# Kernel tuning notes

Hardware: AMD Instinct MI355X
Metric: run time of the kernel (lower is better)

The kernel has to match this reference:

```python
import jax, jax.numpy as jnp
import numpy as np

D_MODEL = 768
NHEAD = 12
DK = D_MODEL // NHEAD
MAX_DIST = 1000.0
FF = 3072
POS_HIDDEN = 32  # hidden width of the relative-position bias MLP
EPS = 1e-5
B, L = 2, 1024


def setup_inputs() -> dict:
    key = jax.random.key(0)
    ks = jax.random.split(key, 24)

    def lin(k, i, o):  # torch-Linear-like init, stored as (in, out)
        return jax.random.uniform(k, (i, o), jnp.float32, -1.0, 1.0) / np.sqrt(i)

    return {
        "src": jax.random.normal(ks[0], (B, L, D_MODEL), jnp.float32),
        "src_x": jax.random.uniform(ks[1], (B, L), jnp.float32) * 1000.0,
        "src_y": jax.random.uniform(ks[2], (B, L), jnp.float32) * 1000.0,
        # attention projections (q,k,v,out)
        "Wq": lin(ks[3], D_MODEL, D_MODEL), "bq": jnp.zeros((D_MODEL,), jnp.float32),
        "Wk": lin(ks[4], D_MODEL, D_MODEL), "bk": jnp.zeros((D_MODEL,), jnp.float32),
        "Wv": lin(ks[5], D_MODEL, D_MODEL), "bv": jnp.zeros((D_MODEL,), jnp.float32),
        "Wo": lin(ks[6], D_MODEL, D_MODEL), "bo": jnp.zeros((D_MODEL,), jnp.float32),
        # relative-position bias MLP: 2 -> POS_HIDDEN -> NHEAD
        "P1": lin(ks[7], 2, POS_HIDDEN), "pb1": jnp.zeros((POS_HIDDEN,), jnp.float32),
        "P2": lin(ks[8], POS_HIDDEN, NHEAD), "pb2": jnp.zeros((NHEAD,), jnp.float32),
        # FFN
        "W1": lin(ks[9], D_MODEL, FF), "b1": jnp.zeros((FF,), jnp.float32),
        "W2": lin(ks[10], FF, D_MODEL), "b2": jnp.zeros((D_MODEL,), jnp.float32),
        # post-LN params
        "g1": jnp.ones((D_MODEL,), jnp.float32), "be1": jnp.zeros((D_MODEL,), jnp.float32),
        "g2": jnp.ones((D_MODEL,), jnp.float32), "be2": jnp.zeros((D_MODEL,), jnp.float32),
    }


def _layernorm(x, g, b):
    m = jnp.mean(x, axis=-1, keepdims=True)
    v = jnp.var(x, axis=-1, keepdims=True)
    return (x - m) * jax.lax.rsqrt(v + EPS) * g + b


def reference(src, src_x, src_y, Wq, bq, Wk, bk, Wv, bv, Wo, bo,
              P1, pb1, P2, pb2, W1, b1, W2, b2, g1, be1, g2, be2):
    b, l, _ = src.shape
    # projections -> (b, h, l, dk)
    q = (src @ Wq + bq).reshape(b, l, NHEAD, DK).transpose(0, 2, 1, 3)
    k = (src @ Wk + bk).reshape(b, l, NHEAD, DK).transpose(0, 2, 1, 3)
    v = (src @ Wv + bv).reshape(b, l, NHEAD, DK).transpose(0, 2, 1, 3)
    # 2D relative positions, clipped and normalized to [-1, 1]
    rx = jnp.clip(src_x[:, :, None] - src_x[:, None, :], -MAX_DIST, MAX_DIST) / MAX_DIST
    ry = jnp.clip(src_y[:, :, None] - src_y[:, None, :], -MAX_DIST, MAX_DIST) / MAX_DIST
    rel = jnp.stack([rx, ry], axis=-1)                        # (b, l, l, 2)
    bias = jax.nn.relu(rel @ P1 + pb1) @ P2 + pb2             # (b, l, l, h)
    bias = bias.transpose(0, 3, 1, 2)                         # (b, h, l, l)
    scores = jnp.einsum('bhqd,bhkd->bhqk', q, k) / np.sqrt(DK).astype(np.float32) + bias
    attn = jax.nn.softmax(scores, axis=-1)
    o = jnp.einsum('bhqk,bhkd->bhqd', attn, v).transpose(0, 2, 1, 3).reshape(b, l, D_MODEL)
    src2 = o @ Wo + bo
    x = _layernorm(src + src2, g1, be1)                       # post-LN residual 1
    ff = jax.nn.relu(x @ W1 + b1) @ W2 + b2                   # FFN
    return _layernorm(x + ff, g2, be2)                        # post-LN residual 2
```

## Files before the change

kernel.cpp:

```cpp
#include <hip/hip_runtime.h>
#include <math.h>

typedef unsigned short ushort_t;
typedef __attribute__((ext_vector_type(8))) short bf16x8;
typedef __attribute__((ext_vector_type(4))) float f32x4;

constexpr int kD      = 768;
constexpr int kNH     = 12;
constexpr int kDK     = 64;
constexpr int kFF     = 3072;
constexpr int kL      = 1024;
constexpr int kRows   = 2048;
constexpr float kEPS  = 1e-5f;

__device__ __forceinline__ ushort_t f2bf(float f) {
    union { float f; unsigned u; } v; v.f = f;
    unsigned r = (v.u + 0x7fffu + ((v.u >> 16) & 1u)) >> 16;
    return (ushort_t)r;
}
__device__ __forceinline__ float bf2f(ushort_t u) {
    union { unsigned u; float f; } v; v.u = ((unsigned)u) << 16; return v.f;
}

#define GL_LDS(gp, lp) __builtin_amdgcn_global_load_lds( \
    (const __attribute__((address_space(1))) void*)(gp), \
    (__attribute__((address_space(3))) void*)(lp), 16, 0, 0)

template<int RELU, int OUTBF, int ADDBIAS>
__device__ __forceinline__ void gemm_body(const ushort_t* __restrict__ A,
                                          const ushort_t* __restrict__ WT,
                                          const float* __restrict__ bias,
                                          void* __restrict__ Cout,
                                          int N, int K, int row0, int col0,
                                          int kbeg, int kend, ushort_t* lds)
{
    ushort_t* As = lds;
    ushort_t* Bs = lds + 4096;

    const int tid  = threadIdx.x;
    const int lane = tid & 63;
    const int wave = tid >> 6;
    const int wrow = (wave & 1) * 64;
    const int wcol = (wave >> 1) * 64;

    const int srow = wave * 16 + (lane >> 2);
    const int sk   = (lane & 3) * 8;
    const ushort_t* ga0 = A  + (size_t)(row0 + srow)      * K + sk;
    const ushort_t* ga1 = A  + (size_t)(row0 + srow + 64) * K + sk;
    const ushort_t* gb0 = WT + (size_t)(col0 + srow)      * K + sk;
    const ushort_t* gb1 = WT + (size_t)(col0 + srow + 64) * K + sk;
    ushort_t* la0 = As + wave * 512;
    ushort_t* la1 = As + 2048 + wave * 512;
    ushort_t* lb0 = Bs + wave * 512;
    ushort_t* lb1 = Bs + 2048 + wave * 512;

    const int fl = lane & 15, fq = lane >> 4;
    const ushort_t* fa[4];
    const ushort_t* fb[4];
    #pragma unroll
    for (int i = 0; i < 4; ++i) {
        fa[i] = As + (wrow + i * 16 + fl) * 32 + fq * 8;
        fb[i] = Bs + (wcol + i * 16 + fl) * 32 + fq * 8;
    }

    f32x4 acc[4][4] = {};

    for (int k0 = kbeg; k0 < kend; k0 += 32) {
        __syncthreads();
        GL_LDS(ga0 + k0, la0);
        GL_LDS(ga1 + k0, la1);
        GL_LDS(gb0 + k0, lb0);
        GL_LDS(gb1 + k0, lb1);
        __syncthreads();

        bf16x8 av[4], bv[4];
        #pragma unroll
        for (int i = 0; i < 4; ++i) {
            av[i] = *(const bf16x8*)fa[i];
            bv[i] = *(const bf16x8*)fb[i];
        }
        #pragma unroll
        for (int mi = 0; mi < 4; ++mi)
            #pragma unroll
            for (int ni = 0; ni < 4; ++ni)
                acc[mi][ni] = __builtin_amdgcn_mfma_f32_16x16x32_bf16(
                    av[mi], bv[ni], acc[mi][ni], 0, 0, 0);
    }

    #pragma unroll
    for (int mi = 0; mi < 4; ++mi) {
        const int m = wrow + mi * 16 + fq * 4;
        #pragma unroll
        for (int ni = 0; ni < 4; ++ni) {
            const int n = wcol + ni * 16 + fl;
            const float bb = ADDBIAS ? bias[col0 + n] : 0.f;
            #pragma unroll
            for (int r = 0; r < 4; ++r) {
                float v = acc[mi][ni][r] + bb;
                if (RELU) v = fmaxf(v, 0.f);
                const size_t idx = (size_t)(row0 + m + r) * N + col0 + n;
                if (OUTBF) ((ushort_t*)Cout)[idx] = f2bf(v);
                else       ((float*)Cout)[idx]    = v;
            }
        }
    }
}

template<int RELU, int OUTBF>
__global__ __launch_bounds__(256)
void gemm_kernel(const ushort_t* __restrict__ A, const ushort_t* __restrict__ WT,
                 const float* __restrict__ bias, void* __restrict__ Cout,
                 int N, int K)
{
    __shared__ ushort_t lds[8192];
    gemm_body<RELU, OUTBF, 1>(A, WT, bias, Cout, N, K,
                              blockIdx.y * 128, blockIdx.x * 128, 0, K, lds);
}

__global__ __launch_bounds__(256)
void gemm_splitk_kernel(const ushort_t* __restrict__ A, const ushort_t* __restrict__ WT,
                        float* __restrict__ parts, int N, int K, int kslice)
{
    __shared__ ushort_t lds[8192];
    const int z = blockIdx.z;
    float* out = parts + (size_t)z * kRows * N;
    gemm_body<0, 0, 0>(A, WT, nullptr, out, N, K,
                       blockIdx.y * 128, blockIdx.x * 128,
                       z * kslice, (z + 1) * kslice, lds);
}

__device__ __forceinline__ void wt_tile(const float* __restrict__ src,
                                        ushort_t* __restrict__ dst,
                                        int K, int N, int kt, int nt,
                                        float (*T)[65], int tid)
{
    #pragma unroll
    for (int i = 0; i < 4; ++i) {
        const int e = tid + i * 256;
        const int r = e >> 4;
        const int c = (e & 15) * 4;
        const float4 f = *(const float4*)&src[(size_t)(kt + r) * N + nt + c];
        T[c + 0][r] = f.x; T[c + 1][r] = f.y; T[c + 2][r] = f.z; T[c + 3][r] = f.w;
    }
    __syncthreads();
    #pragma unroll
    for (int i = 0; i < 4; ++i) {
        const int e = tid + i * 256;
        const int n = e >> 4;
        const int kc = (e & 15) * 4;
        ushort4 o;
        o.x = f2bf(T[n][kc + 0]); o.y = f2bf(T[n][kc + 1]);
        o.z = f2bf(T[n][kc + 2]); o.w = f2bf(T[n][kc + 3]);
        *(ushort4*)&dst[(size_t)(nt + n) * K + kt + kc] = o;
    }
}

__global__ __launch_bounds__(256)
void prep_kernel(const float* __restrict__ Wq, const float* __restrict__ Wk,
                 const float* __restrict__ Wv,
                 ushort_t* wqT, ushort_t* wkT, ushort_t* wvT,
                 const float* __restrict__ src, ushort_t* __restrict__ sb)
{
    __shared__ float T[64][65];
    const int bid = blockIdx.x;
    const int tid = threadIdx.x;

    if (bid < 432) {
        const int wz = bid / 144, t = bid - wz * 144;
        const float* s = (wz == 0) ? Wq : (wz == 1) ? Wk : Wv;
        ushort_t*   d = (wz == 0) ? wqT : (wz == 1) ? wkT : wvT;
        wt_tile(s, d, kD, kD, (t % 12) * 64, (t / 12) * 64, T, tid);
    } else {
        const int i = (bid - 432) * 256 + tid;
        const float4 f = ((const float4*)src)[i];
        ushort4 o;
        o.x = f2bf(f.x); o.y = f2bf(f.y); o.z = f2bf(f.z); o.w = f2bf(f.w);
        ((ushort4*)sb)[i] = o;
    }
}

struct BiasSmem {
    float P[32][16];
    float pb2l[12];
    float qxl[16], qyl[16], kxl[64], kyl[64];
    ushort_t Btile[12 * 1024];
};
struct AttnSmem {
    ushort_t Sp[4][16][72];
    ushort_t Ob[4][16][64];
    float    Ll[4][16];
};

__device__ __forceinline__ void bias_body(int bid, BiasSmem& S,
                 const float* __restrict__ sx, const float* __restrict__ sy,
                 const float* __restrict__ P1, const float* __restrict__ pb1,
                 const float* __restrict__ P2, const float* __restrict__ pb2,
                 ushort_t* __restrict__ biasb)
{
    const int b  = bid >> 10;
    const int qt = (bid >> 4) & 63;
    const int kt = bid & 15;
    const int tid = threadIdx.x;

    if (tid < 32) {
        S.P[tid][0] = P1[tid];
        S.P[tid][1] = P1[32 + tid];
        S.P[tid][2] = pb1[tid];
        S.P[tid][3] = 0.f;
    }
    for (int e = tid; e < 384; e += 256) S.P[e / 12][4 + e % 12] = P2[e];
    if (tid < 12) S.pb2l[tid] = pb2[tid];
    if (tid < 16) { S.qxl[tid] = sx[b * kL + qt * 16 + tid];
                    S.qyl[tid] = sy[b * kL + qt * 16 + tid]; }
    if (tid < 64) { S.kxl[tid] = sx[b * kL + kt * 64 + tid];
                    S.kyl[tid] = sy[b * kL + kt * 64 + tid]; }
    __syncthreads();

    const int ri = tid >> 4;
    const int fl = tid & 15;
    const int fq = ri >> 2, r = ri & 3;
    const int lane16 = fq * 16 + fl;
    const float xi = S.qxl[ri], yi = S.qyl[ri];

    float rx[4], ry[4];
    #pragma unroll
    for (int n = 0; n < 4; ++n) {
        const int cj = n * 16 + fl;
        rx[n] = fminf(fmaxf(xi - S.kxl[cj], -1000.f), 1000.f) * 1e-3f;
        ry[n] = fminf(fmaxf(yi - S.kyl[cj], -1000.f), 1000.f) * 1e-3f;
    }

    float acc[4][12] = {};
    #pragma unroll 4
    for (int u = 0; u < 32; ++u) {
        const float4 pc = *(const float4*)&S.P[u][0];
        const float4 w0 = *(const float4*)&S.P[u][4];
        const float4 w1 = *(const float4*)&S.P[u][8];
        const float4 w2 = *(const float4*)&S.P[u][12];
        float t[4];
        #pragma unroll
        for (int n = 0; n < 4; ++n)
            t[n] = fmaxf(fmaf(rx[n], pc.x, fmaf(ry[n], pc.y, pc.z)), 0.f);
        #pragma unroll
        for (int n = 0; n < 4; ++n) {
            acc[n][0]  = fmaf(t[n], w0.x, acc[n][0]);
            acc[n][1]  = fmaf(t[n], w0.y, acc[n][1]);
            acc[n][2]  = fmaf(t[n], w0.z, acc[n][2]);
            acc[n][3]  = fmaf(t[n], w0.w, acc[n][3]);
            acc[n][4]  = fmaf(t[n], w1.x, acc[n][4]);
            acc[n][5]  = fmaf(t[n], w1.y, acc[n][5]);
            acc[n][6]  = fmaf(t[n], w1.z, acc[n][6]);
            acc[n][7]  = fmaf(t[n], w1.w, acc[n][7]);
            acc[n][8]  = fmaf(t[n], w2.x, acc[n][8]);
            acc[n][9]  = fmaf(t[n], w2.y, acc[n][9]);
            acc[n][10] = fmaf(t[n], w2.z, acc[n][10]);
            acc[n][11] = fmaf(t[n], w2.w, acc[n][11]);
        }
    }

    #pragma unroll
    for (int h = 0; h < 12; ++h) {
        const float pb = S.pb2l[h] - 4.0f;
        #pragma unroll
        for (int n = 0; n < 4; ++n)
            S.Btile[h * 1024 + lane16 * 16 + n * 4 + r] = f2bf(acc[n][h] + pb);
    }
    __syncthreads();

    #pragma unroll
    for (int i = 0; i < 6; ++i) {
        const int off = (i * 256 + tid) * 8;
        const int h = off >> 10;
        const int inner = off & 1023;
        ushort_t* dst = biasb +
            (((size_t)(b * kNH + h) * 64 + qt) * 16 + kt) * 1024 + inner;
        *(uint4*)dst = *(const uint4*)&S.Btile[off];
    }
}

__global__ __launch_bounds__(256)
void qkv_bias_kernel(const ushort_t* __restrict__ A,
                     const ushort_t* wq, const ushort_t* wk, const ushort_t* wv,
                     const float* bq, const float* bk, const float* bv,
                     ushort_t* q, ushort_t* k, ushort_t* v,
                     const float* __restrict__ sx, const float* __restrict__ sy,
                     const float* __restrict__ P1, const float* __restrict__ pb1,
                     const float* __restrict__ P2, const float* __restrict__ pb2,
                     ushort_t* __restrict__ biasb)
{
    __shared__ __align__(16) char smem[sizeof(BiasSmem)];
    const int bid = blockIdx.x;

    if (bid < 288) {
        const int z = bid / 96, rem = bid - z * 96;
        const int bx = rem % 6, by = rem / 6;
        const ushort_t* WT; const float* bias; ushort_t* out;
        if (z == 0)      { WT = wq; bias = bq; out = q; }
        else if (z == 1) { WT = wk; bias = bk; out = k; }
        else             { WT = wv; bias = bv; out = v; }
        gemm_body<0, 1, 1>(A, WT, bias, out, kD, kD,
                           by * 128, bx * 128, 0, kD, (ushort_t*)smem);
    } else {
        bias_body(bid - 288, *(BiasSmem*)smem, sx, sy, P1, pb1, P2, pb2, biasb);
    }
}

__global__ __launch_bounds__(256)
void vtrans_kernel(const ushort_t* __restrict__ vb, ushort_t* __restrict__ vt)
{
    const int bh = blockIdx.x;
    const int b = bh / kNH, h = bh - b * kNH;
    const int j0 = blockIdx.y * 64;
    __shared__ ushort_t T[64][72];

    const int tid = threadIdx.x;
    {
        const int jr = tid & 63;
        const int c0 = (tid >> 6) * 16;
        const ushort_t* sp = vb + (size_t)(b * kL + j0 + jr) * kD + h * kDK + c0;
        uint4 u0 = *(const uint4*)sp;
        uint4 u1 = *(const uint4*)(sp + 8);
        const ushort_t* e0 = (const ushort_t*)&u0;
        const ushort_t* e1 = (const ushort_t*)&u1;
        #pragma unroll
        for (int jj = 0; jj < 8; ++jj) {
            T[c0 + jj][jr]     = e0[jj];
            T[c0 + 8 + jj][jr] = e1[jj];
        }
    }
    __syncthreads();
    {
        const int dr = tid >> 2;
        const int jc = (tid & 3) * 16;
        ushort_t* dp = vt + (size_t)(bh * 64 + dr) * kL + j0 + jc;
        *(uint4*)dp       = *(const uint4*)&T[dr][jc];
        *(uint4*)(dp + 8) = *(const uint4*)&T[dr][jc + 8];
    }
}

constexpr size_t kAttnWtSmem =
    sizeof(AttnSmem) > sizeof(float) * 64 * 65 ? sizeof(AttnSmem)
                                               : sizeof(float) * 64 * 65;

__global__ __launch_bounds__(256)
void attn_wt_kernel(const ushort_t* __restrict__ qg, const ushort_t* __restrict__ kg,
                    const ushort_t* __restrict__ vt, const ushort_t* __restrict__ biasb,
                    ushort_t* __restrict__ og,
                    const float* __restrict__ Wo, const float* __restrict__ W1,
                    const float* __restrict__ W2,
                    ushort_t* woT, ushort_t* w1T, ushort_t* w2T)
{
    __shared__ __align__(16) char smem[kAttnWtSmem];
    const int bid = blockIdx.x;
    const int tid = threadIdx.x;

    if (bid >= 768) {
        float (*T)[65] = (float(*)[65])smem;
        const int t = bid - 768;
        if (t < 144)      wt_tile(Wo, woT, kD,  kD,  (t % 12) * 64, (t / 12) * 64, T, tid);
        else if (t < 720) { const int t2 = t - 144;
                            wt_tile(W1, w1T, kD,  kFF, (t2 % 12) * 64, (t2 / 12) * 64, T, tid); }
        else              { const int t2 = t - 720;
                            wt_tile(W2, w2T, kFF, kD,  (t2 % 48) * 64, (t2 / 48) * 64, T, tid); }
        return;
    }

    AttnSmem& S = *(AttnSmem*)smem;
    const int swz  = (bid & 7) * 96 + (bid >> 3);
    const int bh   = swz >> 5;
    const int qt32 = swz & 31;
    const int b  = bh / kNH, h = bh - b * kNH;
    const int z  = tid >> 6;
    const int qs = z & 1;
    const int kh = z >> 1;
    const int lane = tid & 63;
    const int fl = lane & 15, fq = lane >> 4;
    const int qt = qt32 * 2 + qs;
    const int q0 = qt * 16;
    const int kbeg = kh * 512;

    const size_t qoff = (size_t)(b * kL + q0 + fl) * kD + h * kDK + fq * 8;
    const bf16x8 aq0 = *(const bf16x8*)(qg + qoff);
    const bf16x8 aq1 = *(const bf16x8*)(qg + qoff + 32);

    const ushort_t* kbase = kg + (size_t)(b * kL) * kD + h * kDK + fq * 8;
    const ushort_t* vbase = vt + (size_t)(bh * 64) * kL + fq * 8;
    const ushort_t* btile = biasb +
        ((size_t)(bh * 64 + qt) * 16 + kh * 8) * 1024 + lane * 16;

    f32x4 accO[4] = {};
    float l_part[4] = {};

    bf16x8 kc[4][2];
    uint4 bc0, bc1;
    {
        #pragma unroll
        for (int n = 0; n < 4; ++n) {
            const ushort_t* kr = kbase + (size_t)(kbeg + n * 16 + fl) * kD;
            kc[n][0] = *(const bf16x8*)kr;
            kc[n][1] = *(const bf16x8*)(kr + 32);
        }
        bc0 = *(const uint4*)btile;
        bc1 = *(const uint4*)(btile + 8);
    }

    #pragma unroll 4
    for (int t = 0; t < 8; ++t) {
        const int k0 = kbeg + t * 64;

        bf16x8 vv[4][2];
        #pragma unroll
        for (int n = 0; n < 4; ++n) {
            const ushort_t* vr = vbase + (size_t)(n * 16 + fl) * kL + k0;
            vv[n][0] = *(const bf16x8*)vr;
            vv[n][1] = *(const bf16x8*)(vr + 32);
        }

        f32x4 Sv[4] = {};
        #pragma unroll
        for (int n = 0; n < 4; ++n) {
            Sv[n] = __builtin_amdgcn_mfma_f32_16x16x32_bf16(aq0, kc[n][0], Sv[n], 0, 0, 0);
            Sv[n] = __builtin_amdgcn_mfma_f32_16x16x32_bf16(aq1, kc[n][1], Sv[n], 0, 0, 0);
        }

        bf16x8 kn[4][2];
        uint4 bn0, bn1;
        if (t < 7) {
            #pragma unroll
            for (int n = 0; n < 4; ++n) {
                const ushort_t* kr = kbase + (size_t)(k0 + 64 + n * 16 + fl) * kD;
                kn[n][0] = *(const bf16x8*)kr;
                kn[n][1] = *(const bf16x8*)(kr + 32);
            }
            bn0 = *(const uint4*)(btile + (t + 1) * 1024);
            bn1 = *(const uint4*)(btile + (t + 1) * 1024 + 8);
        }

        ushort_t bu[16];
        *(uint4*)&bu[0] = bc0;
        *(uint4*)&bu[8] = bc1;

        #pragma unroll
        for (int n = 0; n < 4; ++n)
            #pragma unroll
            for (int r = 0; r < 4; ++r) {
                const float e = __expf(fmaf(Sv[n][r], 0.125f, bf2f(bu[n * 4 + r])));
                Sv[n][r] = e;
                l_part[r] += e;
            }

        #pragma unroll
        for (int n = 0; n < 4; ++n)
            #pragma unroll
            for (int r = 0; r < 4; ++r)
                S.Sp[z][fq * 4 + r][n * 16 + fl] = f2bf(Sv[n][r]);

        const bf16x8 ap0 = *(const bf16x8*)&S.Sp[z][fl][fq * 8];
        const bf16x8 ap1 = *(const bf16x8*)&S.Sp[z][fl][32 + fq * 8];
        #pragma unroll
        for (int n = 0; n < 4; ++n) {
            accO[n] = __builtin_amdgcn_mfma_f32_16x16x32_bf16(ap0, vv[n][0], accO[n], 0, 0, 0);
            accO[n] = __builtin_amdgcn_mfma_f32_16x16x32_bf16(ap1, vv[n][1], accO[n], 0, 0, 0);
        }

        if (t < 7) {
            #pragma unroll
            for (int n = 0; n < 4; ++n) { kc[n][0] = kn[n][0]; kc[n][1] = kn[n][1]; }
            bc0 = bn0; bc1 = bn1;
        }
    }

    float l_full[4], inv[4];
    #pragma unroll
    for (int r = 0; r < 4; ++r) {
        float l = l_part[r];
        l += __shfl_xor(l, 1, 16);
        l += __shfl_xor(l, 2, 16);
        l += __shfl_xor(l, 4, 16);
        l += __shfl_xor(l, 8, 16);
        l_full[r] = l;
        inv[r] = 1.0f / l;
    }

    #pragma unroll
    for (int n = 0; n < 4; ++n)
        #pragma unroll
        for (int r = 0; r < 4; ++r)
            S.Ob[z][fq * 4 + r][n * 16 + fl] = f2bf(accO[n][r] * inv[r]);
    if (fl == 0) {
        #pragma unroll
        for (int r = 0; r < 4; ++r)
            S.Ll[z][fq * 4 + r] = l_full[r];
    }
    __syncthreads();

    {
        const int ri = tid >> 3;
        const int d0 = (tid & 7) * 8;
        const int qs2 = ri >> 4, rr = ri & 15;
        const int z0 = qs2, z1 = 2 + qs2;
        const float w0 = S.Ll[z0][rr], w1 = S.Ll[z1][rr];
        const float winv = 1.0f / (w0 + w1);
        const float c0 = w0 * winv, c1 = w1 * winv;

        ushort_t o[8];
        #pragma unroll
        for (int j = 0; j < 8; ++j)
            o[j] = f2bf(fmaf(c0, bf2f(S.Ob[z0][rr][d0 + j]),
                             c1 * bf2f(S.Ob[z1][rr][d0 + j])));
        ushort_t* dp = og + (size_t)(b * kL + qt32 * 32 + ri) * kD + h * kDK + d0;
        *(uint4*)dp = *(const uint4*)o;
    }
}

template<int NPART, int DUAL>
__global__ __launch_bounds__(256)
void ln_kernel(const float* __restrict__ a, const float* __restrict__ parts,
               const float* __restrict__ bias,
               const float* __restrict__ g, const float* __restrict__ be,
               float* __restrict__ out, ushort_t* __restrict__ out_bf)
{
    const int row = blockIdx.x;
    const int tid = threadIdx.x;
    const float* pa = a + (size_t)row * kD;
    constexpr size_t NTOK = (size_t)kRows * kD;

    float v[3];
    float s = 0.f, sq = 0.f;
    #pragma unroll
    for (int i = 0; i < 3; ++i) {
        const int d = tid + i * 256;
        float t = pa[d] + bias[d];
        #pragma unroll
        for (int p = 0; p < NPART; ++p)
            t += parts[p * NTOK + (size_t)row * kD + d];
        v[i] = t;
        s  += t;
        sq += t * t;
    }
    #pragma unroll
    for (int off = 32; off > 0; off >>= 1) {
        s  += __shfl_down(s, off);
        sq += __shfl_down(sq, off);
    }
    __shared__ float bs[4], bq2[4];
    if ((tid & 63) == 0) { bs[tid >> 6] = s; bq2[tid >> 6] = sq; }
    __syncthreads();
    const float ts = bs[0] + bs[1] + bs[2] + bs[3];
    const float tq = bq2[0] + bq2[1] + bq2[2] + bq2[3];
    const float invn = 1.0f / (float)kD;
    const float mean = ts * invn;
    const float var  = tq * invn - mean * mean;
    const float rstd = rsqrtf(var + kEPS);

    float* po = out + (size_t)row * kD;
    #pragma unroll
    for (int i = 0; i < 3; ++i) {
        const int d = tid + i * 256;
        const float o = (v[i] - mean) * rstd * g[d] + be[d];
        po[d] = o;
        if (DUAL) out_bf[(size_t)row * kD + d] = f2bf(o);
    }
}

extern "C" void kernel_launch(void* const* d_in, const int* in_sizes, int n_in,
                              void* d_out, int out_size, void* d_ws, size_t ws_size,
                              hipStream_t stream)
{
    const float* src = (const float*)d_in[0];
    const float* sx  = (const float*)d_in[1];
    const float* sy  = (const float*)d_in[2];
    const float* Wq  = (const float*)d_in[3];  const float* bq  = (const float*)d_in[4];
    const float* Wk  = (const float*)d_in[5];  const float* bk  = (const float*)d_in[6];
    const float* Wv  = (const float*)d_in[7];  const float* bv  = (const float*)d_in[8];
    const float* Wo  = (const float*)d_in[9];  const float* bo  = (const float*)d_in[10];
    const float* P1  = (const float*)d_in[11]; const float* pb1 = (const float*)d_in[12];
    const float* P2  = (const float*)d_in[13]; const float* pb2 = (const float*)d_in[14];
    const float* W1  = (const float*)d_in[15]; const float* b1  = (const float*)d_in[16];
    const float* W2  = (const float*)d_in[17]; const float* b2  = (const float*)d_in[18];
    const float* g1  = (const float*)d_in[19]; const float* be1 = (const float*)d_in[20];
    const float* g2  = (const float*)d_in[21]; const float* be2 = (const float*)d_in[22];

    constexpr size_t W768  = 768u * 768u;
    constexpr size_t W3072 = 768u * 3072u;
    constexpr size_t NTOK  = (size_t)kRows * kD;

    ushort_t* wsu = (ushort_t*)d_ws;
    ushort_t* wqT = wsu;
    ushort_t* wkT = wqT + W768;
    ushort_t* wvT = wkT + W768;
    ushort_t* qb  = wvT + W768;
    ushort_t* kb  = qb + NTOK;
    ushort_t* vb  = kb + NTOK;
    ushort_t* sb  = vb + NTOK;
    ushort_t* vtb = sb + NTOK;
    ushort_t* biasb = vtb + NTOK;
    ushort_t* woT   = biasb;
    ushort_t* w1T   = woT + W768;
    ushort_t* w2T   = w1T + W3072;
    float*    xb    = (float*)(w2T + W3072);
    ushort_t* h1bf  = (ushort_t*)(xb + NTOK);
    float*    s2p   = (float*)h1bf;
    float*    ff2p  = (float*)(h1bf + 4 * NTOK);
    ushort_t* xbf   = qb;

    const dim3 blk(256);

    prep_kernel<<<dim3(1968), blk, 0, stream>>>(Wq, Wk, Wv, wqT, wkT, wvT, src, sb);

    qkv_bias_kernel<<<dim3(2336), blk, 0, stream>>>(
        sb, wqT, wkT, wvT, bq, bk, bv, qb, kb, vb,
        sx, sy, P1, pb1, P2, pb2, biasb);

    vtrans_kernel<<<dim3(2 * kNH, kL / 64), blk, 0, stream>>>(vb, vtb);

    attn_wt_kernel<<<dim3(2064), blk, 0, stream>>>(
        qb, kb, vtb, biasb, sb, Wo, W1, W2,
        (ushort_t*)(ff2p + 3 * NTOK),
        (ushort_t*)(ff2p + 3 * NTOK) + W768,
        (ushort_t*)(ff2p + 3 * NTOK) + W768 + W3072);

    ushort_t* woT2 = (ushort_t*)(ff2p + 3 * NTOK);
    ushort_t* w1T2 = woT2 + W768;
    ushort_t* w2T2 = w1T2 + W3072;

    gemm_splitk_kernel<<<dim3(kD / 128, kRows / 128, 2), blk, 0, stream>>>(
        sb, woT2, s2p, kD, kD, kD / 2);

    ln_kernel<2, 1><<<dim3(kRows), blk, 0, stream>>>(src, s2p, bo, g1, be1, xb, xbf);

    gemm_kernel<1, 1><<<dim3(kFF / 128, kRows / 128), blk, 0, stream>>>(
        xbf, w1T2, b1, h1bf, kFF, kD);

    gemm_splitk_kernel<<<dim3(kD / 128, kRows / 128, 3), blk, 0, stream>>>(
        h1bf, w2T2, ff2p, kD, kFF, kFF / 3);

    ln_kernel<3, 0><<<dim3(kRows), blk, 0, stream>>>(xb, ff2p, b2, g2, be2,
                                                     (float*)d_out, nullptr);
}
```

Baseline: 288.7 us.

## Double-buffer GEMM LDS tiles and raise wave priority around attention MFMAs

The shared GEMM body now prefetches the next K-slice into a second LDS buffer while MFMAs run on the current one, replacing two barriers per iteration with one. LDS allocations double to 32 KB in the GEMM kernels and the fused QKV/bias kernel, which can lower occupancy. The attention kernel also wraps its MFMA blocks in s_setprio to favour matrix issue over other waves.

```diff
diff --git a/kernel.cpp b/kernel.cpp
--- a/kernel.cpp
+++ b/kernel.cpp
@@ -34,9 +34,6 @@
                                           int N, int K, int row0, int col0,
                                           int kbeg, int kend, ushort_t* lds)
 {
-    ushort_t* As = lds;
-    ushort_t* Bs = lds + 4096;
-
     const int tid  = threadIdx.x;
     const int lane = tid & 63;
     const int wave = tid >> 6;
@@ -49,35 +46,39 @@
     const ushort_t* ga1 = A  + (size_t)(row0 + srow + 64) * K + sk;
     const ushort_t* gb0 = WT + (size_t)(col0 + srow)      * K + sk;
     const ushort_t* gb1 = WT + (size_t)(col0 + srow + 64) * K + sk;
-    ushort_t* la0 = As + wave * 512;
-    ushort_t* la1 = As + 2048 + wave * 512;
-    ushort_t* lb0 = Bs + wave * 512;
-    ushort_t* lb1 = Bs + 2048 + wave * 512;
+
+    const int wo = wave * 512;
 
     const int fl = lane & 15, fq = lane >> 4;
-    const ushort_t* fa[4];
-    const ushort_t* fb[4];
-    #pragma unroll
-    for (int i = 0; i < 4; ++i) {
-        fa[i] = As + (wrow + i * 16 + fl) * 32 + fq * 8;
-        fb[i] = Bs + (wcol + i * 16 + fl) * 32 + fq * 8;
-    }
 
     f32x4 acc[4][4] = {};
 
+    {
+        ushort_t* b0 = lds;
+        GL_LDS(ga0 + kbeg, b0 + wo);
+        GL_LDS(ga1 + kbeg, b0 + 2048 + wo);
+        GL_LDS(gb0 + kbeg, b0 + 4096 + wo);
+        GL_LDS(gb1 + kbeg, b0 + 4096 + 2048 + wo);
+    }
+    __syncthreads();
+
+    int cur = 0;
     for (int k0 = kbeg; k0 < kend; k0 += 32) {
-        __syncthreads();
-        GL_LDS(ga0 + k0, la0);
-        GL_LDS(ga1 + k0, la1);
-        GL_LDS(gb0 + k0, lb0);
-        GL_LDS(gb1 + k0, lb1);
-        __syncthreads();
+        ushort_t* bs = lds + (cur ? 8192 : 0);
+        ushort_t* bn = lds + (cur ? 0 : 8192);
+
+        if (k0 + 32 < kend) {
+            GL_LDS(ga0 + k0 + 32, bn + wo);
+            GL_LDS(ga1 + k0 + 32, bn + 2048 + wo);
+            GL_LDS(gb0 + k0 + 32, bn + 4096 + wo);
+            GL_LDS(gb1 + k0 + 32, bn + 4096 + 2048 + wo);
+        }
 
         bf16x8 av[4], bv[4];
         #pragma unroll
         for (int i = 0; i < 4; ++i) {
-            av[i] = *(const bf16x8*)fa[i];
-            bv[i] = *(const bf16x8*)fb[i];
+            av[i] = *(const bf16x8*)(bs + (wrow + i * 16 + fl) * 32 + fq * 8);
+            bv[i] = *(const bf16x8*)(bs + 4096 + (wcol + i * 16 + fl) * 32 + fq * 8);
         }
         #pragma unroll
         for (int mi = 0; mi < 4; ++mi)
@@ -85,6 +86,9 @@
             for (int ni = 0; ni < 4; ++ni)
                 acc[mi][ni] = __builtin_amdgcn_mfma_f32_16x16x32_bf16(
                     av[mi], bv[ni], acc[mi][ni], 0, 0, 0);
+
+        __syncthreads();
+        cur ^= 1;
     }
 
     #pragma unroll
@@ -112,7 +116,7 @@
                  const float* __restrict__ bias, void* __restrict__ Cout,
                  int N, int K)
 {
-    __shared__ ushort_t lds[8192];
+    __shared__ ushort_t lds[16384];
     gemm_body<RELU, OUTBF, 1>(A, WT, bias, Cout, N, K,
                               blockIdx.y * 128, blockIdx.x * 128, 0, K, lds);
 }
@@ -121,7 +125,7 @@
 void gemm_splitk_kernel(const ushort_t* __restrict__ A, const ushort_t* __restrict__ WT,
                         float* __restrict__ parts, int N, int K, int kslice)
 {
-    __shared__ ushort_t lds[8192];
+    __shared__ ushort_t lds[16384];
     const int z = blockIdx.z;
     float* out = parts + (size_t)z * kRows * N;
     gemm_body<0, 0, 0>(A, WT, nullptr, out, N, K,
@@ -278,6 +282,9 @@
     }
 }
 
+constexpr size_t kQkvSmem =
+    sizeof(BiasSmem) > 32768 ? sizeof(BiasSmem) : 32768;
+
 __global__ __launch_bounds__(256)
 void qkv_bias_kernel(const ushort_t* __restrict__ A,
                      const ushort_t* wq, const ushort_t* wk, const ushort_t* wv,
@@ -288,7 +295,7 @@
                      const float* __restrict__ P2, const float* __restrict__ pb2,
                      ushort_t* __restrict__ biasb)
 {
-    __shared__ __align__(16) char smem[sizeof(BiasSmem)];
+    __shared__ __align__(16) char smem[kQkvSmem];
     const int bid = blockIdx.x;
 
     if (bid < 288) {
@@ -417,11 +424,13 @@
         }
 
         f32x4 Sv[4] = {};
+        __builtin_amdgcn_s_setprio(1);
         #pragma unroll
         for (int n = 0; n < 4; ++n) {
             Sv[n] = __builtin_amdgcn_mfma_f32_16x16x32_bf16(aq0, kc[n][0], Sv[n], 0, 0, 0);
             Sv[n] = __builtin_amdgcn_mfma_f32_16x16x32_bf16(aq1, kc[n][1], Sv[n], 0, 0, 0);
         }
+        __builtin_amdgcn_s_setprio(0);
 
         bf16x8 kn[4][2];
         uint4 bn0, bn1;
@@ -457,11 +466,13 @@
 
         const bf16x8 ap0 = *(const bf16x8*)&S.Sp[z][fl][fq * 8];
         const bf16x8 ap1 = *(const bf16x8*)&S.Sp[z][fl][32 + fq * 8];
+        __builtin_amdgcn_s_setprio(1);
         #pragma unroll
         for (int n = 0; n < 4; ++n) {
             accO[n] = __builtin_amdgcn_mfma_f32_16x16x32_bf16(ap0, vv[n][0], accO[n], 0, 0, 0);
             accO[n] = __builtin_amdgcn_mfma_f32_16x16x32_bf16(ap1, vv[n][1], accO[n], 0, 0, 0);
         }
+        __builtin_amdgcn_s_setprio(0);
 
         if (t < 7) {
             #pragma unroll
```

Result: faster. 277.1 us (-4.0%).
